# Optimization experiments

Hardware: AMD Instinct MI355X
Metric: run time of the kernel (lower is better)

Reference implementation:

```python
import jax, jax.numpy as jnp
import numpy as np

TAU = 2.0          # LIF tau
V_TH = 1.0         # threshold, v_reset = 0
EPS = 1e-5         # BN eps
NUM_HEADS = 12
PATCH = 4
LENTH = 64         # (H/p)*(W/p)


def _heaviside(x):
    return (x >= 0.0).astype(x.dtype)


def lif(x_seq):
    """Multi-step LIF (decay_input=True, hard reset to 0). x_seq: [T, ...] -> spikes [T, ...]."""
    def step(v, x):
        v = v + (x - v) / TAU
        s = _heaviside(v - V_TH)
        v = v * (1.0 - s)
        return v, s
    _, s_seq = jax.lax.scan(step, jnp.zeros_like(x_seq[0]), x_seq)
    return s_seq


def bn_eval(x, gamma, beta, mean, var):
    # x: [T,B,C,H,W]; eval-mode BN over channel axis 2
    sh = (1, 1, -1, 1, 1)
    inv = gamma.reshape(sh) / jnp.sqrt(var.reshape(sh) + EPS)
    return (x - mean.reshape(sh)) * inv + beta.reshape(sh)


def setup_inputs() -> dict:
    key = jax.random.key(0)
    ks = jax.random.split(key, 8)
    T, B, C, H, W = 4, 8, 384, 32, 32
    p = PATCH
    x = jax.random.normal(ks[0], (T, B, C, H, W), jnp.float32)
    w_conv = jax.random.normal(ks[1], (2 * C, C, p, p), jnp.float32) / np.sqrt(C * p * p)
    w_proj = jax.random.normal(ks[2], (C, C), jnp.float32) / np.sqrt(C)
    bn1_gamma = 0.5 + jax.random.uniform(ks[3], (2 * C,), jnp.float32)
    bn1_beta = 0.1 * jax.random.normal(ks[4], (2 * C,), jnp.float32)
    bn1_mean = 0.1 * jax.random.normal(ks[5], (2 * C,), jnp.float32)
    bn1_var = 0.5 + jax.random.uniform(ks[6], (2 * C,), jnp.float32)
    bn2_gamma = 0.5 + jax.random.uniform(jax.random.fold_in(key, 10), (C,), jnp.float32)
    bn2_beta = 0.1 * jax.random.normal(jax.random.fold_in(key, 11), (C,), jnp.float32)
    bn2_mean = 0.1 * jax.random.normal(jax.random.fold_in(key, 12), (C,), jnp.float32)
    bn2_var = 0.5 + jax.random.uniform(jax.random.fold_in(key, 13), (C,), jnp.float32)
    fr_x = 0.05 + 0.5 * jax.random.uniform(jax.random.fold_in(key, 14), (1, 1, NUM_HEADS, 1, 1), jnp.float32)
    fr_attn = 0.05 + 0.5 * jax.random.uniform(jax.random.fold_in(key, 15), (1, 1, NUM_HEADS, 1, 1), jnp.float32)
    return dict(x=x, w_conv=w_conv, bn1_gamma=bn1_gamma, bn1_beta=bn1_beta,
                bn1_mean=bn1_mean, bn1_var=bn1_var, w_proj=w_proj,
                bn2_gamma=bn2_gamma, bn2_beta=bn2_beta, bn2_mean=bn2_mean,
                bn2_var=bn2_var, fr_x=fr_x, fr_attn=fr_attn)


def reference(x, w_conv, bn1_gamma, bn1_beta, bn1_mean, bn1_var, w_proj,
              bn2_gamma, bn2_beta, bn2_mean, bn2_var, fr_x, fr_attn):
    T, B, C, H, W = x.shape
    h = NUM_HEADS
    Ch = C // h
    p = PATCH
    x_feat = x
    xs = lif(x)                                           # [T,B,C,H,W] spikes
    # patchify conv (kernel=stride=p, no bias), flatten T*B for the conv
    y = jax.lax.conv_general_dilated(
        xs.reshape(T * B, C, H, W), w_conv, (p, p), 'VALID',
        dimension_numbers=('NCHW', 'OIHW', 'NCHW'))
    Hp, Wp = H // p, W // p
    y = bn_eval(y.reshape(T, B, 2 * C, Hp, Wp), bn1_gamma, bn1_beta, bn1_mean, bn1_var)
    y = y.reshape(T, B, h, 2 * Ch, Hp * Wp)
    y1, y2 = y[:, :, :, :Ch, :], y[:, :, :, Ch:, :]       # [T,B,h,Ch,N']
    xr = xs.reshape(T, B, h, Ch, H * W)                   # [T,B,h,Ch,N]
    scale1 = 1.0 / jnp.sqrt(fr_x * Ch)                    # [1,1,h,1,1]
    attn = jnp.einsum('tbhdp,tbhdn->tbhpn', y1, xr) * scale1   # [T,B,h,N',N]
    attn = lif(attn)
    scale2 = 1.0 / jnp.sqrt(fr_attn * LENTH)
    out = jnp.einsum('tbhdp,tbhpn->tbhdn', y2, attn) * scale2  # [T,B,h,Ch,N]
    out = lif(out.reshape(T, B, C, H, W))
    out = jnp.einsum('tbchw,oc->tbohw', out, w_proj)      # 1x1 conv, no bias
    out = bn_eval(out, bn2_gamma, bn2_beta, bn2_mean, bn2_var)
    return out + x_feat
```

## Files before the change

### kernel.cpp

```cpp
#include <hip/hip_runtime.h>
#include <math.h>

#define TT 4
#define BB 8
#define CC 384
#define HWN 1024
#define NHEAD 12
#define CHD 32
#define C2 768
#define LL 64
#define KCONV 6144
#define KB_TOT 192
#define MROWS 2048

#define K2INV ((_Float16)4.8828125e-4f)

typedef _Float16 f16x8 __attribute__((ext_vector_type(8)));
typedef _Float16 f16x4 __attribute__((ext_vector_type(4)));
typedef float f32x4 __attribute__((ext_vector_type(4)));

#if defined(__has_builtin)
#if __has_builtin(__builtin_amdgcn_global_load_lds)
#define USE_GLL 1
#endif
#endif
#ifndef USE_GLL
#define USE_GLL 0
#endif

#if USE_GLL
typedef __attribute__((address_space(3))) unsigned int lds_uint;
typedef const __attribute__((address_space(1))) unsigned int glob_uint;
__device__ __forceinline__ void load_lds16(const void* g, void* l) {
    __builtin_amdgcn_global_load_lds((glob_uint*)g, (lds_uint*)l, 16, 0, 0);
}
#endif

__global__ __launch_bounds__(256) void k_pack(const float* __restrict__ w,
                                              _Float16* __restrict__ W0,
                                              _Float16* __restrict__ W1) {
    __shared__ __align__(16) _Float16 Lh[4096];
    __shared__ __align__(16) _Float16 Ll[4096];
    int kb = blockIdx.x, nb = blockIdx.y;
    int tid = threadIdx.x;
    int r0 = tid >> 3;
    int c4 = (tid & 7) * 4;
    int q = c4 >> 3, j0 = c4 & 7;
#pragma unroll
    for (int ri = 0; ri < 4; ri++) {
        int col = ri * 32 + r0;
        const float* src = w + (size_t)(nb * 128 + col) * KCONV + kb * 32 + c4;
        float4 v = *(const float4*)src;
        float vv[4] = {v.x, v.y, v.z, v.w};
#pragma unroll
        for (int e = 0; e < 4; e++) {
            _Float16 h = (_Float16)vv[e];
            float rem = (vv[e] - (float)h) * 2048.0f;
            Lh[q * 1024 + col * 8 + j0 + e] = h;
            Ll[q * 1024 + col * 8 + j0 + e] = (_Float16)rem;
        }
    }
    __syncthreads();
    size_t o = ((size_t)kb * 6 + nb) * 4096 + tid * 16;
    *(f16x8*)(W0 + o) = *(const f16x8*)&Lh[tid * 16];
    *(f16x8*)(W0 + o + 8) = *(const f16x8*)&Lh[tid * 16 + 8];
    *(f16x8*)(W1 + o) = *(const f16x8*)&Ll[tid * 16];
    *(f16x8*)(W1 + o + 8) = *(const f16x8*)&Ll[tid * 16 + 8];
}

__global__ __launch_bounds__(256) void k_pack_wp(const float* __restrict__ wp,
                                                 _Float16* __restrict__ WpH) {
    __shared__ __align__(16) _Float16 Lh[4096];
    int kb = blockIdx.x, ot = blockIdx.y;
    int tid = threadIdx.x;
    int r0 = tid >> 3;
    int c4 = (tid & 7) * 4;
    int q = c4 >> 3, j0 = c4 & 7;
#pragma unroll
    for (int ri = 0; ri < 4; ri++) {
        int col = ri * 32 + r0;
        const float* src = wp + (size_t)(ot * 128 + col) * CC + kb * 32 + c4;
        float4 v = *(const float4*)src;
        float vv[4] = {v.x, v.y, v.z, v.w};
#pragma unroll
        for (int e = 0; e < 4; e++)
            Lh[q * 1024 + col * 8 + j0 + e] = (_Float16)vv[e];
    }
    __syncthreads();
    size_t o = ((size_t)kb * 3 + ot) * 4096 + tid * 16;
    *(f16x8*)(WpH + o) = *(const f16x8*)&Lh[tid * 16];
    *(f16x8*)(WpH + o + 8) = *(const f16x8*)&Lh[tid * 16 + 8];
}

__global__ __launch_bounds__(256) void k_lif1(const float* __restrict__ x,
                                              _Float16* __restrict__ xsC,
                                              _Float16* __restrict__ xsF) {
    int nt = blockIdx.x & 3, q8 = blockIdx.x >> 2;
    int bh = blockIdx.y;
    int b = bh / NHEAD, hh = bh % NHEAD;
    int n = nt * 256 + threadIdx.x;
    const int stride = BB * CC * HWN;
    int h = n >> 5, w = n & 31;
    int pi = h >> 2, a = h & 3, pj = w >> 2, bp = w & 3;
    int rowp = pi * 8 + pj;
    int qa = a >> 1;
    int jc = (a & 1) * 4 + bp;
    size_t base0 = ((size_t)b * CC + hh * 32 + q8 * 8) * HWN + n;
    f16x8 frag[4];
#pragma unroll
    for (int j = 0; j < 8; j++) {
        int c = hh * 32 + q8 * 8 + j;
        int kb = c >> 1;
        int qc = (c & 1) * 2 + qa;
        size_t cbase = (size_t)kb * 4096 + qc * 1024 + jc;
        float v = 0.0f;
        size_t off = base0 + (size_t)j * HWN;
#pragma unroll
        for (int t = 0; t < TT; t++) {
            float xv = x[(size_t)t * stride + off];
            v += (xv - v) * 0.5f;
            float s = (v >= 1.0f) ? 1.0f : 0.0f;
            if (s > 0.0f) v = 0.0f;
            frag[t][j] = (_Float16)s;
            int tb = t * BB + b;
            int mt = tb >> 1;
            int row = (tb & 1) * 64 + rowp;
            xsC[(size_t)mt * (192 * 4096) + cbase + (size_t)row * 8] = (_Float16)s;
        }
    }
#pragma unroll
    for (int t = 0; t < TT; t++) {
        int tb = t * BB + b;
        size_t dst = ((size_t)(tb * NHEAD + hh) * 8 + (n >> 7)) * 4096 + q8 * 1024 + (size_t)(n & 127) * 8;
        *(f16x8*)(xsF + dst) = frag[t];
    }
}

__global__ __launch_bounds__(256, 3) void k_conv_mfma(const _Float16* __restrict__ xsC,
                                                      const _Float16* __restrict__ W0,
                                                      const _Float16* __restrict__ W1,
                                                      float* __restrict__ P,
                                                      int KS, int kbPerSplit) {
    __shared__ __align__(16) _Float16 As[2][4096];
    __shared__ __align__(16) _Float16 Bh[2][4096];
    __shared__ __align__(16) _Float16 Bl[2][4096];

    int bid = blockIdx.x;
    int s = bid % KS;
    int idx = bid / KS;
    int mt = idx & 15;
    int nt = idx >> 4;
    int kb0 = s * kbPerSplit;
    int tid = threadIdx.x;
    int wave = tid >> 6;
    int lane = tid & 63;
    int l16 = lane & 15, lq = lane >> 4;
    int wr = (wave & 1) * 64, wc = (wave >> 1) * 64;

    f32x4 acc[4][4];
#pragma unroll
    for (int i = 0; i < 4; i++)
#pragma unroll
        for (int j = 0; j < 4; j++) acc[i][j] = (f32x4){0.f, 0.f, 0.f, 0.f};

    const char* aBase = (const char*)xsC + (size_t)mt * (192 * 8192);
    const char* b0Base = (const char*)W0 + (size_t)nt * 8192;
    const char* b1Base = (const char*)W1 + (size_t)nt * 8192;
    int wo = wave * 2048;
    int lo16 = lane * 16;

#if USE_GLL
#define STAGE(buf, kb) do {                                              \
    const char* aS = aBase + (size_t)(kb) * 8192;                        \
    const char* b0S = b0Base + (size_t)(kb) * (6 * 8192);                \
    const char* b1S = b1Base + (size_t)(kb) * (6 * 8192);                \
    load_lds16(aS + wo + lo16, (char*)As[buf] + wo);                     \
    load_lds16(aS + wo + 1024 + lo16, (char*)As[buf] + wo + 1024);       \
    load_lds16(b0S + wo + lo16, (char*)Bh[buf] + wo);                    \
    load_lds16(b0S + wo + 1024 + lo16, (char*)Bh[buf] + wo + 1024);      \
    load_lds16(b1S + wo + lo16, (char*)Bl[buf] + wo);                    \
    load_lds16(b1S + wo + 1024 + lo16, (char*)Bl[buf] + wo + 1024);      \
} while (0)
#else
#define STAGE(buf, kb) do {                                              \
    const char* aS = aBase + (size_t)(kb) * 8192;                        \
    const char* b0S = b0Base + (size_t)(kb) * (6 * 8192);                \
    const char* b1S = b1Base + (size_t)(kb) * (6 * 8192);                \
    _Pragma("unroll")                                                    \
    for (int i_ = 0; i_ < 2; ++i_) {                                     \
        int off_ = wo + i_ * 1024 + lo16;                                \
        *(float4*)((char*)As[buf] + off_) = *(const float4*)(aS + off_); \
        *(float4*)((char*)Bh[buf] + off_) = *(const float4*)(b0S + off_);\
        *(float4*)((char*)Bl[buf] + off_) = *(const float4*)(b1S + off_);\
    }                                                                    \
} while (0)
#endif

    STAGE(0, kb0);
    __syncthreads();

    int cur = 0;
    for (int i = 0; i < kbPerSplit; ++i) {
        if (i + 1 < kbPerSplit) STAGE(cur ^ 1, kb0 + i + 1);

        f16x8 wf[4], sf[4], sfs[4];
#pragma unroll
        for (int fj = 0; fj < 4; fj++) {
            sf[fj] = *(const f16x8*)&As[cur][(size_t)(lq * 128 + wr + fj * 16 + l16) * 8];
            sfs[fj] = sf[fj] * K2INV;
        }
#pragma unroll
        for (int fi = 0; fi < 4; fi++)
            wf[fi] = *(const f16x8*)&Bh[cur][(size_t)(lq * 128 + wc + fi * 16 + l16) * 8];
#pragma unroll
        for (int fi = 0; fi < 4; fi++)
#pragma unroll
            for (int fj = 0; fj < 4; fj++)
                acc[fi][fj] = __builtin_amdgcn_mfma_f32_16x16x32_f16(wf[fi], sf[fj], acc[fi][fj], 0, 0, 0);
#pragma unroll
        for (int fi = 0; fi < 4; fi++)
            wf[fi] = *(const f16x8*)&Bl[cur][(size_t)(lq * 128 + wc + fi * 16 + l16) * 8];
#pragma unroll
        for (int fi = 0; fi < 4; fi++)
#pragma unroll
            for (int fj = 0; fj < 4; fj++)
                acc[fi][fj] = __builtin_amdgcn_mfma_f32_16x16x32_f16(wf[fi], sfs[fj], acc[fi][fj], 0, 0, 0);

        __syncthreads();
        cur ^= 1;
    }
#undef STAGE

    size_t Pbase = (size_t)s * MROWS * C2;
#pragma unroll
    for (int fi = 0; fi < 4; fi++) {
        int oc0 = nt * 128 + wc + fi * 16 + lq * 4;
#pragma unroll
        for (int fj = 0; fj < 4; fj++) {
            int m = mt * 128 + wr + fj * 16 + l16;
            *(f32x4*)(P + Pbase + (size_t)m * C2 + oc0) = acc[fi][fj];
        }
    }
}

__global__ __launch_bounds__(256) void k_reduce_frag(const float* __restrict__ P,
                                                     const float* __restrict__ g1,
                                                     const float* __restrict__ b1,
                                                     const float* __restrict__ m1,
                                                     const float* __restrict__ v1,
                                                     _Float16* __restrict__ A1,
                                                     _Float16* __restrict__ A2,
                                                     int KS) {
    __shared__ float y2ls[32][66];
    int tb = blockIdx.x / NHEAD, hh = blockIdx.x % NHEAD;
    int tid = threadIdx.x;
    int pp = tid >> 2, cq = (tid & 3) * 16;

    size_t rowbase = ((size_t)tb * 64 + pp) * C2 + hh * 64 + cq;
    float yv[16];
#pragma unroll
    for (int i = 0; i < 16; i++) yv[i] = 0.0f;
    for (int s = 0; s < KS; s++) {
        const float* p = P + (size_t)s * MROWS * C2 + rowbase;
#pragma unroll
        for (int i4 = 0; i4 < 4; i4++) {
            float4 v = *(const float4*)(p + i4 * 4);
            yv[i4 * 4 + 0] += v.x;
            yv[i4 * 4 + 1] += v.y;
            yv[i4 * 4 + 2] += v.z;
            yv[i4 * 4 + 3] += v.w;
        }
    }
#pragma unroll
    for (int i = 0; i < 16; i++) {
        int oc = hh * 64 + cq + i;
        float inv = g1[oc] / sqrtf(v1[oc] + 1e-5f);
        yv[i] = (yv[i] - m1[oc]) * inv + b1[oc];
    }

    size_t reg = (size_t)(tb * NHEAD + hh) * 4096;
    if (cq < 32) {
#pragma unroll
        for (int gi = 0; gi < 2; gi++) {
            int c0 = cq + gi * 8;
            f16x8 h, l;
#pragma unroll
            for (int j = 0; j < 8; j++) {
                float v = yv[gi * 8 + j];
                _Float16 hi = (_Float16)v;
                h[j] = hi;
                l[j] = (_Float16)((v - (float)hi) * 2048.0f);
            }
            size_t a = reg + (size_t)(((pp >> 4) * 4 + (c0 >> 3)) * 128 + (pp & 15) * 8);
            *(f16x8*)(A1 + a) = h;
            *(f16x8*)(A1 + a + 2048) = l;
        }
    } else {
#pragma unroll
        for (int i = 0; i < 16; i++) y2ls[cq - 32 + i][pp] = yv[i];
    }
    __syncthreads();
    int d16 = tid & 15, grp = tid >> 4;
    f16x8 h, l;
#pragma unroll
    for (int j = 0; j < 8; j++) {
        float v = y2ls[(grp >> 3) * 16 + d16][((grp >> 2) & 1) * 32 + (grp & 3) * 8 + j];
        _Float16 hi = (_Float16)v;
        h[j] = hi;
        l[j] = (_Float16)((v - (float)hi) * 2048.0f);
    }
    size_t a = reg + (size_t)((grp * 16 + d16) * 8);
    *(f16x8*)(A2 + a) = h;
    *(f16x8*)(A2 + a + 2048) = l;
}

__global__ __launch_bounds__(256, 3) void k_attn_mfma(const _Float16* __restrict__ xsF,
                                                      const _Float16* __restrict__ A1,
                                                      const _Float16* __restrict__ A2,
                                                      const float* __restrict__ fr_x,
                                                      const float* __restrict__ fr_attn,
                                                      _Float16* __restrict__ OsF) {
    __shared__ __align__(16) _Float16 Bs[4][128][8];
    __shared__ __align__(16) _Float16 Sat[8][128][8];

    int nt = blockIdx.x;
    int bh = blockIdx.y;
    int b = bh / NHEAD, hh = bh % NHEAD;
    int tid = threadIdx.x;
    int w = tid >> 6;
    int lane = tid & 63;
    int l16 = lane & 15, lq = lane >> 4;

    float scale1 = 1.0f / sqrtf(fr_x[hh] * 32.0f);
    float scale2 = 1.0f / sqrtf(fr_attn[hh] * 64.0f);

    float va[8][4];
    float vo[2][2][4];
#pragma unroll
    for (int nf = 0; nf < 8; nf++)
#pragma unroll
        for (int r = 0; r < 4; r++) va[nf][r] = 0.0f;
#pragma unroll
    for (int dt = 0; dt < 2; dt++)
#pragma unroll
        for (int nf = 0; nf < 2; nf++)
#pragma unroll
            for (int r = 0; r < 4; r++) vo[dt][nf][r] = 0.0f;

    for (int t = 0; t < TT; t++) {
        int tb = t * BB + b;
        size_t reg = (size_t)(tb * NHEAD + hh);
        const char* src = (const char*)(xsF + (reg * 8 + nt) * 4096);
#if USE_GLL
        load_lds16(src + tid * 16, (char*)&Bs[0][0][0] + tid * 16);
        load_lds16(src + tid * 16 + 4096, (char*)&Bs[0][0][0] + tid * 16 + 4096);
#else
        *(float4*)((char*)&Bs[0][0][0] + tid * 16) = *(const float4*)(src + tid * 16);
        *(float4*)((char*)&Bs[0][0][0] + tid * 16 + 4096) = *(const float4*)(src + tid * 16 + 4096);
#endif
        const _Float16* a1b = A1 + reg * 4096;
        f16x8 a1h = *(const f16x8*)(a1b + (size_t)(((w * 4 + lq) * 16 + l16) * 8));
        f16x8 a1l = *(const f16x8*)(a1b + 2048 + (size_t)(((w * 4 + lq) * 16 + l16) * 8));
        f16x8 a1ls = a1l * K2INV;
        __syncthreads();

        f32x4 ah[8];
#pragma unroll
        for (int nf = 0; nf < 8; nf++) ah[nf] = (f32x4){0.f, 0.f, 0.f, 0.f};
#pragma unroll
        for (int nf = 0; nf < 8; nf++) {
            f16x8 bf = *(const f16x8*)&Bs[lq][nf * 16 + l16][0];
            ah[nf] = __builtin_amdgcn_mfma_f32_16x16x32_f16(a1h, bf, ah[nf], 0, 0, 0);
            ah[nf] = __builtin_amdgcn_mfma_f32_16x16x32_f16(a1ls, bf, ah[nf], 0, 0, 0);
        }
        int pq = w * 2 + (lq >> 1);
#pragma unroll
        for (int nf = 0; nf < 8; nf++) {
            f16x4 sp;
#pragma unroll
            for (int r = 0; r < 4; r++) {
                float a = ah[nf][r] * scale1;
                float v = va[nf][r];
                v += (a - v) * 0.5f;
                float s = (v >= 1.0f) ? 1.0f : 0.0f;
                va[nf][r] = (s > 0.0f) ? 0.0f : v;
                sp[r] = (_Float16)s;
            }
            *(f16x4*)&Sat[pq][nf * 16 + l16][(lq & 1) * 4] = sp;
        }
        __syncthreads();

        const _Float16* a2b = A2 + reg * 4096;
        f32x4 oh[2][2];
#pragma unroll
        for (int dt = 0; dt < 2; dt++)
#pragma unroll
            for (int nf = 0; nf < 2; nf++) oh[dt][nf] = (f32x4){0.f, 0.f, 0.f, 0.f};
#pragma unroll
        for (int ks = 0; ks < 2; ks++) {
            f16x8 bf0 = *(const f16x8*)&Sat[ks * 4 + lq][w * 32 + l16][0];
            f16x8 bf1 = *(const f16x8*)&Sat[ks * 4 + lq][w * 32 + 16 + l16][0];
#pragma unroll
            for (int dt = 0; dt < 2; dt++) {
                size_t ao = (size_t)(((dt * 8 + ks * 4 + lq) * 16 + l16) * 8);
                f16x8 a2h = *(const f16x8*)(a2b + ao);
                f16x8 a2ls = *(const f16x8*)(a2b + 2048 + ao) * K2INV;
                oh[dt][0] = __builtin_amdgcn_mfma_f32_16x16x32_f16(a2h, bf0, oh[dt][0], 0, 0, 0);
                oh[dt][0] = __builtin_amdgcn_mfma_f32_16x16x32_f16(a2ls, bf0, oh[dt][0], 0, 0, 0);
                oh[dt][1] = __builtin_amdgcn_mfma_f32_16x16x32_f16(a2h, bf1, oh[dt][1], 0, 0, 0);
                oh[dt][1] = __builtin_amdgcn_mfma_f32_16x16x32_f16(a2ls, bf1, oh[dt][1], 0, 0, 0);
            }
        }
        _Float16* og = OsF + (reg * 8 + nt) * 4096;
#pragma unroll
        for (int dt = 0; dt < 2; dt++)
#pragma unroll
            for (int nf = 0; nf < 2; nf++) {
                f16x4 sp;
#pragma unroll
                for (int r = 0; r < 4; r++) {
                    float a = oh[dt][nf][r] * scale2;
                    float v = vo[dt][nf][r];
                    v += (a - v) * 0.5f;
                    float s = (v >= 1.0f) ? 1.0f : 0.0f;
                    vo[dt][nf][r] = (s > 0.0f) ? 0.0f : v;
                    sp[r] = (_Float16)s;
                }
                int n = w * 32 + nf * 16 + l16;
                *(f16x4*)(og + (size_t)((dt * 2 + (lq >> 1)) * 1024 + n * 8 + (lq & 1) * 4)) = sp;
            }
        __syncthreads();
    }
}

__global__ __launch_bounds__(256, 3) void k_proj_mfma(const _Float16* __restrict__ OsF,
                                                      const _Float16* __restrict__ WpH,
                                                      const float* __restrict__ g2,
                                                      const float* __restrict__ b2,
                                                      const float* __restrict__ m2,
                                                      const float* __restrict__ vv2,
                                                      const float* __restrict__ x,
                                                      float* __restrict__ out) {
    __shared__ __align__(16) _Float16 Bs[2][4096];

    int bid = blockIdx.x;
    int xcd = bid & 7;
    int idx = bid >> 3;
    int tb = xcd * 4 + idx / 24;
    int rem = idx % 24;
    int nt = rem & 7;
    int ot = rem >> 3;
    int tid = threadIdx.x;
    int wave = tid >> 6;
    int lane = tid & 63;
    int l16 = lane & 15, lq = lane >> 4;
    int wn = (wave & 1) * 64, wo = (wave >> 1) * 64;

    f32x4 acc[4][4];
#pragma unroll
    for (int i = 0; i < 4; i++)
#pragma unroll
        for (int j = 0; j < 4; j++) acc[i][j] = (f32x4){0.f, 0.f, 0.f, 0.f};

    const char* bBase = (const char*)(OsF + ((size_t)tb * NHEAD * 8 + nt) * 4096);
    const _Float16* aBase = WpH + (size_t)ot * 4096 + lq * 1024 + (size_t)(wo + l16) * 8;
    int halfo = wave * 2048;
    int lo16 = lane * 16;

#if USE_GLL
#define PSTAGE(buf, kb) do {                                                   \
    const char* bS = bBase + (size_t)(kb) * (8 * 8192);                        \
    load_lds16(bS + halfo + lo16, (char*)Bs[buf] + halfo);                     \
    load_lds16(bS + halfo + 1024 + lo16, (char*)Bs[buf] + halfo + 1024);       \
} while (0)
#else
#define PSTAGE(buf, kb) do {                                                   \
    const char* bS = bBase + (size_t)(kb) * (8 * 8192);                        \
    _Pragma("unroll")                                                          \
    for (int i_ = 0; i_ < 2; ++i_) {                                           \
        int off_ = halfo + i_ * 1024 + lo16;                                   \
        *(float4*)((char*)Bs[buf] + off_) = *(const float4*)(bS + off_);       \
    }                                                                          \
} while (0)
#endif

    f16x8 af[4], afn[4];
#pragma unroll
    for (int fo = 0; fo < 4; fo++) af[fo] = *(const f16x8*)(aBase + (size_t)(fo * 16) * 8);
    PSTAGE(0, 0);
    __syncthreads();

    int cur = 0;
    for (int kb = 0; kb < 12; ++kb) {
        int kbn = (kb + 1 < 12) ? kb + 1 : kb;
        if (kb + 1 < 12) PSTAGE(cur ^ 1, kb + 1);
        const _Float16* an = aBase + (size_t)kbn * (3 * 4096);
#pragma unroll
        for (int fo = 0; fo < 4; fo++) afn[fo] = *(const f16x8*)(an + (size_t)(fo * 16) * 8);

        f16x8 bf[4];
#pragma unroll
        for (int fn = 0; fn < 4; fn++)
            bf[fn] = *(const f16x8*)&Bs[cur][(size_t)(lq * 128 + wn + fn * 16 + l16) * 8];
#pragma unroll
        for (int fn = 0; fn < 4; fn++)
#pragma unroll
            for (int fo = 0; fo < 4; fo++)
                acc[fn][fo] = __builtin_amdgcn_mfma_f32_16x16x32_f16(bf[fn], af[fo], acc[fn][fo], 0, 0, 0);

        __syncthreads();
        cur ^= 1;
#pragma unroll
        for (int fo = 0; fo < 4; fo++) af[fo] = afn[fo];
    }
#undef PSTAGE

    size_t orow_base = (size_t)tb * CC * HWN;
#pragma unroll
    for (int fo = 0; fo < 4; fo++) {
        int o = ot * 128 + wo + fo * 16 + l16;
        float inv = g2[o] / sqrtf(vv2[o] + 1e-5f);
        float mu = m2[o];
        float bt = b2[o];
        size_t obase = orow_base + (size_t)o * HWN;
#pragma unroll
        for (int fn = 0; fn < 4; fn++) {
            size_t addr = obase + (size_t)(nt * 128 + wn + fn * 16 + lq * 4);
            float4 xv = *(const float4*)(x + addr);
            f32x4 a = acc[fn][fo];
            float4 ov;
            ov.x = (a[0] - mu) * inv + bt + xv.x;
            ov.y = (a[1] - mu) * inv + bt + xv.y;
            ov.z = (a[2] - mu) * inv + bt + xv.z;
            ov.w = (a[3] - mu) * inv + bt + xv.w;
            *(float4*)(out + addr) = ov;
        }
    }
}

extern "C" void kernel_launch(void* const* d_in, const int* in_sizes, int n_in,
                              void* d_out, int out_size, void* d_ws, size_t ws_size,
                              hipStream_t stream) {
    const float* x = (const float*)d_in[0];
    const float* w_conv = (const float*)d_in[1];
    const float* bn1_gamma = (const float*)d_in[2];
    const float* bn1_beta = (const float*)d_in[3];
    const float* bn1_mean = (const float*)d_in[4];
    const float* bn1_var = (const float*)d_in[5];
    const float* w_proj = (const float*)d_in[6];
    const float* bn2_gamma = (const float*)d_in[7];
    const float* bn2_beta = (const float*)d_in[8];
    const float* bn2_mean = (const float*)d_in[9];
    const float* bn2_var = (const float*)d_in[10];
    const float* fr_x = (const float*)d_in[11];
    const float* fr_attn = (const float*)d_in[12];

    const size_t FRAG = (size_t)16 * 192 * 4096 * 2;
    const size_t AB = (size_t)TT * BB * NHEAD * 4096 * 2;
    const size_t WB = (size_t)KCONV * C2 * 2;
    const size_t WPB = (size_t)CC * CC * 2;
    const size_t PB = (size_t)MROWS * C2 * 4;
    _Float16* xsC = (_Float16*)d_ws;
    _Float16* xsF = (_Float16*)((char*)xsC + FRAG);
    _Float16* OsF = (_Float16*)((char*)xsF + FRAG);
    _Float16* A1 = (_Float16*)((char*)OsF + FRAG);
    _Float16* A2 = (_Float16*)((char*)A1 + AB);
    _Float16* W0 = (_Float16*)((char*)A2 + AB);
    _Float16* W1 = (_Float16*)((char*)W0 + WB);
    _Float16* WpH = (_Float16*)((char*)W1 + WB);
    char* tail = (char*)WpH + WPB;

    int KS;
    float* P;
    if (ws_size >= (size_t)(tail - (char*)d_ws) + 8 * PB) {
        KS = 8;
        P = (float*)tail;
    } else if (ws_size >= (size_t)(tail - (char*)d_ws) + 4 * PB) {
        KS = 4;
        P = (float*)tail;
    } else {
        KS = 2;
        P = (float*)OsF;
    }
    int kbPerSplit = KB_TOT / KS;

    k_pack<<<dim3(KB_TOT, 6), 256, 0, stream>>>(w_conv, W0, W1);
    k_pack_wp<<<dim3(12, 3), 256, 0, stream>>>(w_proj, WpH);
    k_lif1<<<dim3(16, BB * NHEAD), 256, 0, stream>>>(x, xsC, xsF);
    k_conv_mfma<<<96 * KS, 256, 0, stream>>>(xsC, W0, W1, P, KS, kbPerSplit);
    k_reduce_frag<<<32 * NHEAD, 256, 0, stream>>>(P, bn1_gamma, bn1_beta, bn1_mean, bn1_var, A1, A2, KS);
    k_attn_mfma<<<dim3(8, BB * NHEAD), 256, 0, stream>>>(xsF, A1, A2, fr_x, fr_attn, OsF);
    k_proj_mfma<<<768, 256, 0, stream>>>(OsF, WpH, bn2_gamma, bn2_beta, bn2_mean, bn2_var, x, (float*)d_out);
}
```

Baseline: 122.9 us.

## Deepen conv GEMM prefetch pipeline and coalesce LIF1 conv-layout stores via LDS

The conv MFMA loop now prefetches two K-blocks ahead with direct global-to-LDS loads. It waits with explicit vmcnt/lgkmcnt counters and raw barriers, and loads all LDS fragments before issuing the prefetch, so global loads overlap more of the MFMA work. Separately, k_lif1 no longer does scattered 2-byte stores into the conv-layout buffer. It stages spikes through shared memory and writes coalesced 16-byte vectors. The hand-written waitcnt counts and sched barriers depend on exact load counts per stage, which is fragile, and the LIF1 change adds syncthreads per timestep.

After: 121.6 us. Within noise of the previous version (-1.1%).

```diff
diff --git a/kernel.cpp b/kernel.cpp
--- a/kernel.cpp
+++ b/kernel.cpp
@@ -23,9 +23,21 @@
 #if __has_builtin(__builtin_amdgcn_global_load_lds)
 #define USE_GLL 1
 #endif
+#if __has_builtin(__builtin_amdgcn_sched_barrier)
+#define HAVE_SCHEDBAR 1
+#endif
 #endif
 #ifndef USE_GLL
 #define USE_GLL 0
+#endif
+#ifndef HAVE_SCHEDBAR
+#define HAVE_SCHEDBAR 0
+#endif
+
+#if HAVE_SCHEDBAR
+#define SCHED_FENCE() __builtin_amdgcn_sched_barrier(0)
+#else
+#define SCHED_FENCE()
 #endif
 
 #if USE_GLL
@@ -95,24 +107,22 @@
 __global__ __launch_bounds__(256) void k_lif1(const float* __restrict__ x,
                                               _Float16* __restrict__ xsC,
                                               _Float16* __restrict__ xsF) {
+    __shared__ __align__(16) _Float16 S[4][4][16][8];
     int nt = blockIdx.x & 3, q8 = blockIdx.x >> 2;
     int bh = blockIdx.y;
     int b = bh / NHEAD, hh = bh % NHEAD;
-    int n = nt * 256 + threadIdx.x;
+    int tid = threadIdx.x;
+    int n = nt * 256 + tid;
     const int stride = BB * CC * HWN;
     int h = n >> 5, w = n & 31;
-    int pi = h >> 2, a = h & 3, pj = w >> 2, bp = w & 3;
-    int rowp = pi * 8 + pj;
+    int a = h & 3, pj = w >> 2, bp = w & 3;
     int qa = a >> 1;
     int jc = (a & 1) * 4 + bp;
+    int rowloc = ((h >> 2) & 1) * 8 + pj;
     size_t base0 = ((size_t)b * CC + hh * 32 + q8 * 8) * HWN + n;
     f16x8 frag[4];
 #pragma unroll
     for (int j = 0; j < 8; j++) {
-        int c = hh * 32 + q8 * 8 + j;
-        int kb = c >> 1;
-        int qc = (c & 1) * 2 + qa;
-        size_t cbase = (size_t)kb * 4096 + qc * 1024 + jc;
         float v = 0.0f;
         size_t off = base0 + (size_t)j * HWN;
 #pragma unroll
@@ -122,10 +132,6 @@
             float s = (v >= 1.0f) ? 1.0f : 0.0f;
             if (s > 0.0f) v = 0.0f;
             frag[t][j] = (_Float16)s;
-            int tb = t * BB + b;
-            int mt = tb >> 1;
-            int row = (tb & 1) * 64 + rowp;
-            xsC[(size_t)mt * (192 * 4096) + cbase + (size_t)row * 8] = (_Float16)s;
         }
     }
 #pragma unroll
@@ -133,6 +139,21 @@
         int tb = t * BB + b;
         size_t dst = ((size_t)(tb * NHEAD + hh) * 8 + (n >> 7)) * 4096 + q8 * 1024 + (size_t)(n & 127) * 8;
         *(f16x8*)(xsF + dst) = frag[t];
+    }
+    int kb0 = hh * 16 + q8 * 4;
+    int okb = tid >> 6, oqc = (tid >> 4) & 3, orow = tid & 15;
+#pragma unroll
+    for (int t = 0; t < TT; t++) {
+        __syncthreads();
+#pragma unroll
+        for (int j = 0; j < 8; j++)
+            S[j >> 1][(j & 1) * 2 + qa][rowloc][jc] = frag[t][j];
+        __syncthreads();
+        int tb = t * BB + b;
+        int mt = tb >> 1;
+        int row = (tb & 1) * 64 + nt * 16 + orow;
+        _Float16* dst = xsC + (size_t)mt * (192 * 4096) + (size_t)(kb0 + okb) * 4096 + oqc * 1024 + (size_t)row * 8;
+        *(f16x8*)dst = *(const f16x8*)&S[okb][oqc][orow][0];
     }
 }
 
@@ -181,6 +202,50 @@
     load_lds16(b1S + wo + lo16, (char*)Bl[buf] + wo);                    \
     load_lds16(b1S + wo + 1024 + lo16, (char*)Bl[buf] + wo + 1024);      \
 } while (0)
+
+    STAGE(0, kb0);
+    if (kbPerSplit > 1) STAGE(1, kb0 + 1);
+    int cur = 0;
+    for (int i = 0; i < kbPerSplit; ++i) {
+        if (i < kbPerSplit - 1)
+            asm volatile("s_waitcnt vmcnt(6)" ::: "memory");
+        else
+            asm volatile("s_waitcnt vmcnt(0)" ::: "memory");
+        __builtin_amdgcn_s_barrier();
+        SCHED_FENCE();
+
+        f16x8 wfh[4], wfl[4], sf[4], sfs[4];
+#pragma unroll
+        for (int fj = 0; fj < 4; fj++)
+            sf[fj] = *(const f16x8*)&As[cur][(size_t)(lq * 128 + wr + fj * 16 + l16) * 8];
+#pragma unroll
+        for (int fi = 0; fi < 4; fi++) {
+            wfh[fi] = *(const f16x8*)&Bh[cur][(size_t)(lq * 128 + wc + fi * 16 + l16) * 8];
+            wfl[fi] = *(const f16x8*)&Bl[cur][(size_t)(lq * 128 + wc + fi * 16 + l16) * 8];
+        }
+        asm volatile("s_waitcnt lgkmcnt(0)" ::: "memory");
+        SCHED_FENCE();
+        __builtin_amdgcn_s_barrier();
+        SCHED_FENCE();
+        if (i + 2 < kbPerSplit) STAGE(cur, kb0 + i + 2);
+        SCHED_FENCE();
+
+#pragma unroll
+        for (int fj = 0; fj < 4; fj++) sfs[fj] = sf[fj] * K2INV;
+#pragma unroll
+        for (int fi = 0; fi < 4; fi++)
+#pragma unroll
+            for (int fj = 0; fj < 4; fj++)
+                acc[fi][fj] = __builtin_amdgcn_mfma_f32_16x16x32_f16(wfh[fi], sf[fj], acc[fi][fj], 0, 0, 0);
+#pragma unroll
+        for (int fi = 0; fi < 4; fi++)
+#pragma unroll
+            for (int fj = 0; fj < 4; fj++)
+                acc[fi][fj] = __builtin_amdgcn_mfma_f32_16x16x32_f16(wfl[fi], sfs[fj], acc[fi][fj], 0, 0, 0);
+
+        cur ^= 1;
+    }
+#undef STAGE
 #else
 #define STAGE(buf, kb) do {                                              \
     const char* aS = aBase + (size_t)(kb) * 8192;                        \
@@ -194,42 +259,37 @@
         *(float4*)((char*)Bl[buf] + off_) = *(const float4*)(b1S + off_);\
     }                                                                    \
 } while (0)
-#endif
-
     STAGE(0, kb0);
     __syncthreads();
-
     int cur = 0;
     for (int i = 0; i < kbPerSplit; ++i) {
         if (i + 1 < kbPerSplit) STAGE(cur ^ 1, kb0 + i + 1);
-
-        f16x8 wf[4], sf[4], sfs[4];
+        f16x8 wfh[4], wfl[4], sf[4], sfs[4];
 #pragma unroll
         for (int fj = 0; fj < 4; fj++) {
             sf[fj] = *(const f16x8*)&As[cur][(size_t)(lq * 128 + wr + fj * 16 + l16) * 8];
             sfs[fj] = sf[fj] * K2INV;
         }
 #pragma unroll
+        for (int fi = 0; fi < 4; fi++) {
+            wfh[fi] = *(const f16x8*)&Bh[cur][(size_t)(lq * 128 + wc + fi * 16 + l16) * 8];
+            wfl[fi] = *(const f16x8*)&Bl[cur][(size_t)(lq * 128 + wc + fi * 16 + l16) * 8];
+        }
+#pragma unroll
         for (int fi = 0; fi < 4; fi++)
-            wf[fi] = *(const f16x8*)&Bh[cur][(size_t)(lq * 128 + wc + fi * 16 + l16) * 8];
+#pragma unroll
+            for (int fj = 0; fj < 4; fj++)
+                acc[fi][fj] = __builtin_amdgcn_mfma_f32_16x16x32_f16(wfh[fi], sf[fj], acc[fi][fj], 0, 0, 0);
 #pragma unroll
         for (int fi = 0; fi < 4; fi++)
 #pragma unroll
             for (int fj = 0; fj < 4; fj++)
-                acc[fi][fj] = __builtin_amdgcn_mfma_f32_16x16x32_f16(wf[fi], sf[fj], acc[fi][fj], 0, 0, 0);
-#pragma unroll
-        for (int fi = 0; fi < 4; fi++)
-            wf[fi] = *(const f16x8*)&Bl[cur][(size_t)(lq * 128 + wc + fi * 16 + l16) * 8];
-#pragma unroll
-        for (int fi = 0; fi < 4; fi++)
-#pragma unroll
-            for (int fj = 0; fj < 4; fj++)
-                acc[fi][fj] = __builtin_amdgcn_mfma_f32_16x16x32_f16(wf[fi], sfs[fj], acc[fi][fj], 0, 0, 0);
-
+                acc[fi][fj] = __builtin_amdgcn_mfma_f32_16x16x32_f16(wfl[fi], sfs[fj], acc[fi][fj], 0, 0, 0);
         __syncthreads();
         cur ^= 1;
     }
 #undef STAGE
+#endif
 
     size_t Pbase = (size_t)s * MROWS * C2;
 #pragma unroll
```
